# Performance work log

Hardware: AMD Instinct MI355X
Metric: run time of the kernel (lower is better)

The kernel has to match this reference:

```python
import jax, jax.numpy as jnp
import numpy as np

B, S, D = 46, 50, 768
GAMA = 1.0 - 2.0 ** -5  # 1 - np.power(2.0, -5 - arange(0,1)) -> scalar 0.96875


def make_pe(n, d):
    # PositionalEncoding buffer pe[:n]; note original adds pe[:emb.size(0)],
    # i.e. the encoding is indexed by BATCH position (faithful to source).
    position = jnp.arange(n, dtype=jnp.float32)[:, None]
    div_term = jnp.exp(jnp.arange(0, d, 2, dtype=jnp.float32) * (-np.log(10000.0) / d))
    pe = jnp.zeros((n, d), dtype=jnp.float32)
    pe = pe.at[:, 0::2].set(jnp.sin(position * div_term))
    pe = pe.at[:, 1::2].set(jnp.cos(position * div_term))
    return pe[:, None, :]  # [n, 1, d] broadcasts over the seq dim


def setup_inputs() -> dict:
    key = jax.random.key(0)
    ks = jax.random.split(key, 6)
    w = lambda k, shape: jax.random.normal(k, shape, dtype=jnp.float32) * 0.02
    return {
        "text_embedding": jax.random.normal(ks[0], (B, S, D), dtype=jnp.float32),
        "embedding": jax.random.normal(ks[1], (B, S, D), dtype=jnp.float32),
        "Wq_w": w(ks[2], (D, D)), "Wq_b": jnp.zeros((D,), jnp.float32),
        "Wk_w": w(ks[3], (D, D)), "Wk_b": jnp.zeros((D,), jnp.float32),
        "Wv_w": w(ks[4], (D, D)), "Wv_b": jnp.zeros((D,), jnp.float32),
        "lin_w": w(ks[5], (S, D)), "lin_b": jnp.zeros((S,), jnp.float32),
    }


def reference(text_embedding, embedding, Wq_w, Wq_b, Wk_w, Wk_b, Wv_w, Wv_b, lin_w, lin_b):
    b = text_embedding.shape[0]
    pe = make_pe(b, D)  # [B,1,D]
    # dropout p=0.1 is identity in eval mode
    Q = text_embedding @ Wq_w.T + Wq_b + pe          # [B,S,D]
    K = embedding @ Wk_w.T + Wk_b + pe               # [B,S,D]
    V = embedding @ Wv_w.T + Wv_b                    # [B,S,D]
    # head_num == 1, so transpose_for_scores is a no-op view
    Q_trans = Q @ lin_w.T + lin_b                    # [B,S,S] (S == 50)
    scores = jnp.einsum('bqd,bkd->bqk', Q, K) * 8.0  # scaling *8 as in source
    probs = jax.nn.softmax(scores, axis=-1)
    ctx = jnp.einsum('bqk,bkd->bqd', probs, V)       # [B,S,D] context_layer

    # RetNet-like gamma-decay recurrence over the batch dim (host-sync loop in
    # the original, expressed here as an on-device lax.scan):
    #   s_i = Q_trans @ (gama * s_{i-1}) + ctx[i],  s_{-1} = 0
    def step(s, c_i):  # s: [B,S,D], c_i: [S,D]
        s_new = jnp.einsum('bij,bjd->bid', Q_trans, GAMA * s) + c_i[None]
        return s_new, s_new
    _, rec = jax.lax.scan(step, jnp.zeros_like(ctx), ctx)  # [B,B,S,D]
    return ctx, rec
```

## Files before the change

### kernel.cpp

```cpp
#include <hip/hip_runtime.h>
#include <math.h>

#define NB 46
#define NS 50
#define ND 768
#define GAMA 0.96875f
#define NM 2300

using bfrag  = __attribute__((ext_vector_type(8))) short;
using f32x16 = __attribute__((ext_vector_type(16))) float;

union FragU { unsigned u[4]; bfrag f; };

__device__ __forceinline__ void cvt_hilo(const float f[8], bfrag& fh, bfrag& fl)
{
    FragU uh, ul;
    #pragma unroll
    for (int t = 0; t < 4; t++) {
        const unsigned b0 = __float_as_uint(f[2 * t]);
        const unsigned b1 = __float_as_uint(f[2 * t + 1]);
        uh.u[t] = (b0 >> 16) | (b1 & 0xFFFF0000u);
        const float r0 = f[2 * t]     - __uint_as_float(b0 & 0xFFFF0000u);
        const float r1 = f[2 * t + 1] - __uint_as_float(b1 & 0xFFFF0000u);
        ul.u[t] = (__float_as_uint(r0) >> 16) | (__float_as_uint(r1) & 0xFFFF0000u);
    }
    fh = uh.f; fl = ul.f;
}

__global__ __launch_bounds__(256) void qkv_gemm(
    const float* __restrict__ text_emb, const float* __restrict__ emb,
    const float* __restrict__ Wq, const float* __restrict__ bq,
    const float* __restrict__ Wk, const float* __restrict__ bk,
    const float* __restrict__ Wv, const float* __restrict__ bv,
    float* __restrict__ Q, float* __restrict__ K, float* __restrict__ V)
{
    const int z = blockIdx.z;
    const float* X    = (z == 0) ? text_emb : emb;
    const float* W    = (z == 0) ? Wq : (z == 1) ? Wk : Wv;
    const float* bias = (z == 0) ? bq : (z == 1) ? bk : bv;
    float* out        = (z == 0) ? Q  : (z == 1) ? K  : V;

    __shared__ float Xs[32][68];
    __shared__ float Ws[32][68];

    const int tid = threadIdx.x;
    const int w   = tid >> 6;
    const int l   = tid & 63;
    const int c   = l & 31;
    const int h   = l >> 5;
    const int wm  = w >> 1, wn = w & 1;
    const int m0  = blockIdx.x * 64, n0 = blockIdx.y * 64;

    const int lrow = tid >> 2;
    const int lk   = (tid & 3) * 4;
    const int xm   = m0 + lrow;
    const float* __restrict__ Xrow = X + (size_t)(xm < NM ? xm : 0) * ND;
    const float* __restrict__ Wrow = W + (size_t)(n0 + lrow) * ND;

    f32x16 acc;
    #pragma unroll
    for (int g = 0; g < 16; g++) acc[g] = 0.f;

    for (int k0 = 0; k0 < ND; k0 += 32) {
        const float4 xv0 = *reinterpret_cast<const float4*>(&Xrow[k0 + lk]);
        const float4 xv1 = *reinterpret_cast<const float4*>(&Xrow[k0 + 16 + lk]);
        const float4 wv0 = *reinterpret_cast<const float4*>(&Wrow[k0 + lk]);
        const float4 wv1 = *reinterpret_cast<const float4*>(&Wrow[k0 + 16 + lk]);
        __syncthreads();
        Xs[lk + 0][lrow] = xv0.x; Xs[lk + 1][lrow] = xv0.y;
        Xs[lk + 2][lrow] = xv0.z; Xs[lk + 3][lrow] = xv0.w;
        Xs[16 + lk + 0][lrow] = xv1.x; Xs[16 + lk + 1][lrow] = xv1.y;
        Xs[16 + lk + 2][lrow] = xv1.z; Xs[16 + lk + 3][lrow] = xv1.w;
        Ws[lk + 0][lrow] = wv0.x; Ws[lk + 1][lrow] = wv0.y;
        Ws[lk + 2][lrow] = wv0.z; Ws[lk + 3][lrow] = wv0.w;
        Ws[16 + lk + 0][lrow] = wv1.x; Ws[16 + lk + 1][lrow] = wv1.y;
        Ws[16 + lk + 2][lrow] = wv1.z; Ws[16 + lk + 3][lrow] = wv1.w;
        __syncthreads();

        #pragma unroll
        for (int kt = 0; kt < 2; kt++) {
            float fx[8], fw[8];
            #pragma unroll
            for (int j = 0; j < 8; j++) {
                fx[j] = Xs[16 * kt + 8 * h + j][32 * wm + c];
                fw[j] = Ws[16 * kt + 8 * h + j][32 * wn + c];
            }
            bfrag Ah, Al, Bh, Bl;
            cvt_hilo(fx, Ah, Al);
            cvt_hilo(fw, Bh, Bl);
            acc = __builtin_amdgcn_mfma_f32_32x32x16_bf16(Ah, Bh, acc, 0, 0, 0);
            acc = __builtin_amdgcn_mfma_f32_32x32x16_bf16(Ah, Bl, acc, 0, 0, 0);
            acc = __builtin_amdgcn_mfma_f32_32x32x16_bf16(Al, Bh, acc, 0, 0, 0);
        }
    }

    const float C2 = -0.0239861701969175f;
    const int n = n0 + 32 * wn + c;
    #pragma unroll
    for (int g = 0; g < 16; g++) {
        const int rr = (g & 3) + 8 * (g >> 2) + 4 * h;
        const int m  = m0 + 32 * wm + rr;
        if (m >= NM) continue;
        float v = acc[g] + bias[n];
        if (z < 2) {
            const int bpos = m / NS;
            const float ang = (float)bpos * expf((float)(n >> 1) * C2);
            v += (n & 1) ? cosf(ang) : sinf(ang);
        }
        out[(size_t)m * ND + n] = v;
    }
}

__global__ __launch_bounds__(256, 1) void attn(
    const float* __restrict__ Q, const float* __restrict__ K,
    const float* __restrict__ V,
    const float* __restrict__ lin_w, const float* __restrict__ lin_b,
    float* __restrict__ Ag, float* __restrict__ ctx_out)
{
    const int b   = blockIdx.x;
    const int tid = threadIdx.x;
    const int w   = tid >> 6;
    const int l   = tid & 63;
    const int c   = l & 31;
    const int h   = l >> 5;

    __shared__ float Lsh[9 * 64 * 68];
    float* SP = Lsh;
    float* QP = Lsh + 4 * 64 * 68;
    float* Pf = Lsh + 8 * 64 * 68;

    const float* __restrict__ Qb = Q + (size_t)b * NS * ND;
    const float* __restrict__ Kb = K + (size_t)b * NS * ND;
    const float* __restrict__ Vb = V + (size_t)b * NS * ND;

    f32x16 accS[2][2], accQ[2][2];
    #pragma unroll
    for (int mt = 0; mt < 2; mt++)
        #pragma unroll
        for (int nt = 0; nt < 2; nt++)
            #pragma unroll
            for (int g = 0; g < 16; g++) { accS[mt][nt][g] = 0.f; accQ[mt][nt][g] = 0.f; }

    const int ks = w * 192;
    for (int kt = 0; kt < 12; ++kt) {
        const int ko = ks + kt * 16 + 8 * h;
        bfrag Qh[2], Ql[2], Kh[2], Kl[2], Wh[2], Wl[2];
        #pragma unroll
        for (int mt = 0; mt < 2; mt++) {
            const int row = 32 * mt + c;
            const int r = (row < NS) ? row : 0;
            float f[8];
            {
                const float4 a0 = *reinterpret_cast<const float4*>(&Qb[(size_t)r * ND + ko]);
                const float4 a1 = *reinterpret_cast<const float4*>(&Qb[(size_t)r * ND + ko + 4]);
                f[0]=a0.x; f[1]=a0.y; f[2]=a0.z; f[3]=a0.w; f[4]=a1.x; f[5]=a1.y; f[6]=a1.z; f[7]=a1.w;
            }
            cvt_hilo(f, Qh[mt], Ql[mt]);
            {
                const float4 a0 = *reinterpret_cast<const float4*>(&Kb[(size_t)r * ND + ko]);
                const float4 a1 = *reinterpret_cast<const float4*>(&Kb[(size_t)r * ND + ko + 4]);
                f[0]=a0.x; f[1]=a0.y; f[2]=a0.z; f[3]=a0.w; f[4]=a1.x; f[5]=a1.y; f[6]=a1.z; f[7]=a1.w;
            }
            cvt_hilo(f, Kh[mt], Kl[mt]);
            {
                const float4 a0 = *reinterpret_cast<const float4*>(&lin_w[(size_t)r * ND + ko]);
                const float4 a1 = *reinterpret_cast<const float4*>(&lin_w[(size_t)r * ND + ko + 4]);
                f[0]=a0.x; f[1]=a0.y; f[2]=a0.z; f[3]=a0.w; f[4]=a1.x; f[5]=a1.y; f[6]=a1.z; f[7]=a1.w;
            }
            cvt_hilo(f, Wh[mt], Wl[mt]);
        }
        #pragma unroll
        for (int mt = 0; mt < 2; mt++)
            #pragma unroll
            for (int nt = 0; nt < 2; nt++) {
                f32x16 a = accS[mt][nt];
                a = __builtin_amdgcn_mfma_f32_32x32x16_bf16(Qh[mt], Kh[nt], a, 0, 0, 0);
                a = __builtin_amdgcn_mfma_f32_32x32x16_bf16(Qh[mt], Kl[nt], a, 0, 0, 0);
                a = __builtin_amdgcn_mfma_f32_32x32x16_bf16(Ql[mt], Kh[nt], a, 0, 0, 0);
                accS[mt][nt] = a;
                f32x16 q = accQ[mt][nt];
                q = __builtin_amdgcn_mfma_f32_32x32x16_bf16(Qh[mt], Wh[nt], q, 0, 0, 0);
                q = __builtin_amdgcn_mfma_f32_32x32x16_bf16(Qh[mt], Wl[nt], q, 0, 0, 0);
                q = __builtin_amdgcn_mfma_f32_32x32x16_bf16(Ql[mt], Wh[nt], q, 0, 0, 0);
                accQ[mt][nt] = q;
            }
    }

    {
        float* SPw = SP + w * (64 * 68);
        float* QPw = QP + w * (64 * 68);
        #pragma unroll
        for (int mt = 0; mt < 2; mt++)
            #pragma unroll
            for (int nt = 0; nt < 2; nt++)
                #pragma unroll
                for (int g = 0; g < 16; g++) {
                    const int rg  = 32 * mt + (g & 3) + 8 * (g >> 2) + 4 * h;
                    const int col = 32 * nt + c;
                    SPw[rg * 68 + col] = accS[mt][nt][g];
                    QPw[rg * 68 + col] = accQ[mt][nt][g];
                }
    }
    __syncthreads();

    {
        const int r  = tid >> 2;
        const int cg = (tid & 3) * 16;
        #pragma unroll
        for (int q4 = 0; q4 < 4; ++q4) {
            const int off = r * 68 + cg + q4 * 4;
            float4 s0 = *reinterpret_cast<const float4*>(&SP[off]);
            float4 s1 = *reinterpret_cast<const float4*>(&SP[64 * 68 + off]);
            float4 s2 = *reinterpret_cast<const float4*>(&SP[2 * 64 * 68 + off]);
            float4 s3 = *reinterpret_cast<const float4*>(&SP[3 * 64 * 68 + off]);
            float4 r4;
            r4.x = 8.f * ((s0.x + s1.x) + (s2.x + s3.x));
            r4.y = 8.f * ((s0.y + s1.y) + (s2.y + s3.y));
            r4.z = 8.f * ((s0.z + s1.z) + (s2.z + s3.z));
            r4.w = 8.f * ((s0.w + s1.w) + (s2.w + s3.w));
            *reinterpret_cast<float4*>(&SP[off]) = r4;
            float4 t0 = *reinterpret_cast<const float4*>(&QP[off]);
            float4 t1 = *reinterpret_cast<const float4*>(&QP[64 * 68 + off]);
            float4 t2 = *reinterpret_cast<const float4*>(&QP[2 * 64 * 68 + off]);
            float4 t3 = *reinterpret_cast<const float4*>(&QP[3 * 64 * 68 + off]);
            float4 u4;
            u4.x = (t0.x + t1.x) + (t2.x + t3.x);
            u4.y = (t0.y + t1.y) + (t2.y + t3.y);
            u4.z = (t0.z + t1.z) + (t2.z + t3.z);
            u4.w = (t0.w + t1.w) + (t2.w + t3.w);
            *reinterpret_cast<float4*>(&QP[off]) = u4;
        }
    }
    __syncthreads();

    if (tid < NS) {
        const float* Sr = SP + tid * 68;
        float mx = -INFINITY;
        for (int c2 = 0; c2 < NS; ++c2) mx = fmaxf(mx, Sr[c2]);
        float sum = 0.f;
        for (int c2 = 0; c2 < NS; ++c2) {
            const float e = expf(Sr[c2] - mx);
            Pf[tid * 68 + c2] = e;
            sum += e;
        }
        const float inv = 1.f / sum;
        for (int c2 = 0; c2 < NS; ++c2) Pf[tid * 68 + c2] *= inv;
        for (int c2 = NS; c2 < 64; ++c2) Pf[tid * 68 + c2] = 0.f;
    }
    for (int e = tid; e < NS * NS; e += 256) {
        const int r = e / NS, cc = e - r * NS;
        Ag[b * (NS * NS) + e] = GAMA * (QP[r * 68 + cc] + lin_b[cc]);
    }
    __syncthreads();

    bfrag Ph[2][4], Pl[2][4];
    #pragma unroll
    for (int mt = 0; mt < 2; mt++)
        #pragma unroll
        for (int kt = 0; kt < 4; kt++) {
            float f[8];
            #pragma unroll
            for (int j = 0; j < 8; j++)
                f[j] = Pf[(32 * mt + c) * 68 + kt * 16 + 8 * h + j];
            cvt_hilo(f, Ph[mt][kt], Pl[mt][kt]);
        }

    for (int j3 = 0; j3 < 3; ++j3) {
        const int dbase = (w * 3 + j3) * 64;
        f32x16 accC[2][2];
        #pragma unroll
        for (int mt = 0; mt < 2; mt++)
            #pragma unroll
            for (int nt = 0; nt < 2; nt++)
                #pragma unroll
                for (int g = 0; g < 16; g++) accC[mt][nt][g] = 0.f;

        #pragma unroll
        for (int nt = 0; nt < 2; nt++) {
            const int d = dbase + 32 * nt + c;
            #pragma unroll
            for (int kt = 0; kt < 4; kt++) {
                float f[8];
                #pragma unroll
                for (int j = 0; j < 8; j++) {
                    const int k2 = kt * 16 + 8 * h + j;
                    f[j] = (k2 < NS) ? Vb[(size_t)k2 * ND + d] : 0.f;
                }
                bfrag Bh, Bl;
                cvt_hilo(f, Bh, Bl);
                #pragma unroll
                for (int mt = 0; mt < 2; mt++) {
                    f32x16 a = accC[mt][nt];
                    a = __builtin_amdgcn_mfma_f32_32x32x16_bf16(Ph[mt][kt], Bh, a, 0, 0, 0);
                    a = __builtin_amdgcn_mfma_f32_32x32x16_bf16(Ph[mt][kt], Bl, a, 0, 0, 0);
                    a = __builtin_amdgcn_mfma_f32_32x32x16_bf16(Pl[mt][kt], Bh, a, 0, 0, 0);
                    accC[mt][nt] = a;
                }
            }
        }
        #pragma unroll
        for (int mt = 0; mt < 2; mt++)
            #pragma unroll
            for (int nt = 0; nt < 2; nt++)
                #pragma unroll
                for (int g = 0; g < 16; g++) {
                    const int rg = 32 * mt + (g & 3) + 8 * (g >> 2) + 4 * h;
                    if (rg < NS)
                        ctx_out[((size_t)b * NS + rg) * ND + dbase + 32 * nt + c] = accC[mt][nt][g];
                }
    }
}

__global__ __launch_bounds__(64, 1) void recur(
    const float* __restrict__ Ag, const float* __restrict__ ctx,
    float* __restrict__ rec)
{
    const int blk   = blockIdx.x;
    const int b     = blk / 24;
    const int chunk = blk - b * 24;
    const int l     = threadIdx.x;
    const int c     = l & 31;
    const int h     = l >> 5;
    const int d0    = chunk * 32;
    const int srow  = l >> 3;
    const int scol  = (l & 7) * 4;

    __shared__ float Sf[64 * 32];
    __shared__ float Cx[64 * 32];

    const float* __restrict__ Ab = Ag + b * (NS * NS);
    bfrag Ah[2][4], Al[2][4];
    #pragma unroll
    for (int mt = 0; mt < 2; mt++) {
        const int row = 32 * mt + c;
        const bool rok = row < NS;
        const float* __restrict__ Arow = Ab + row * NS;
        #pragma unroll
        for (int kt = 0; kt < 4; kt++) {
            FragU uh, ul;
            #pragma unroll
            for (int t = 0; t < 4; t++) {
                const int k0 = 16 * kt + 8 * h + 2 * t;
                const float e = (rok && k0     < NS) ? Arow[k0]     : 0.f;
                const float o = (rok && k0 + 1 < NS) ? Arow[k0 + 1] : 0.f;
                const unsigned ue = __float_as_uint(e), uo = __float_as_uint(o);
                uh.u[t] = (ue >> 16) | (uo & 0xFFFF0000u);
                const float re = e - __uint_as_float(ue & 0xFFFF0000u);
                const float ro = o - __uint_as_float(uo & 0xFFFF0000u);
                ul.u[t] = (__float_as_uint(re) >> 16) | (__float_as_uint(ro) & 0xFFFF0000u);
            }
            Ah[mt][kt] = uh.f; Al[mt][kt] = ul.f;
        }
    }

    {
        const float4 z = make_float4(0.f, 0.f, 0.f, 0.f);
        *reinterpret_cast<float4*>(&Cx[(48 + srow) * 32 + scol]) = z;
        *reinterpret_cast<float4*>(&Cx[(56 + srow) * 32 + scol]) = z;
        *reinterpret_cast<float4*>(&Sf[(48 + srow) * 32 + scol]) = z;
        *reinterpret_cast<float4*>(&Sf[(56 + srow) * 32 + scol]) = z;
    }

    float4 creg[7];
    #pragma unroll
    for (int it = 0; it < 7; ++it) creg[it] = make_float4(0.f, 0.f, 0.f, 0.f);
    {
        const float* __restrict__ src = ctx + d0;
        #pragma unroll
        for (int it = 0; it < 7; ++it) {
            const int r = it * 8 + srow;
            if (r < NS)
                creg[it] = *reinterpret_cast<const float4*>(&src[(size_t)r * ND + scol]);
        }
        float* __restrict__ r0 = rec + (size_t)b * NS * ND + d0;
        #pragma unroll
        for (int it = 0; it < 7; ++it) {
            const int r = it * 8 + srow;
            if (r < NS) {
                *reinterpret_cast<float4*>(&Sf[r * 32 + scol]) = creg[it];
                *reinterpret_cast<float4*>(&r0[(size_t)r * ND + scol]) = creg[it];
            }
        }
    }
    {
        const float* __restrict__ src = ctx + (size_t)NS * ND + d0;
        #pragma unroll
        for (int it = 0; it < 7; ++it) {
            const int r = it * 8 + srow;
            if (r < NS)
                creg[it] = *reinterpret_cast<const float4*>(&src[(size_t)r * ND + scol]);
        }
    }

    for (int i = 1; i < NB; ++i) {
        #pragma unroll
        for (int it = 0; it < 7; ++it) {
            const int r = it * 8 + srow;
            if (r < NS)
                *reinterpret_cast<float4*>(&Cx[r * 32 + scol]) = creg[it];
        }
        if (i + 1 < NB) {
            const float* __restrict__ src = ctx + (size_t)(i + 1) * NS * ND + d0;
            #pragma unroll
            for (int it = 0; it < 7; ++it) {
                const int r = it * 8 + srow;
                if (r < NS)
                    creg[it] = *reinterpret_cast<const float4*>(&src[(size_t)r * ND + scol]);
            }
        }
        f32x16 acc[2];
        #pragma unroll
        for (int mt = 0; mt < 2; mt++)
            #pragma unroll
            for (int g = 0; g < 16; g++) {
                const int rg = 32 * mt + (g & 3) + 8 * (g >> 2) + 4 * h;
                acc[mt][g] = Cx[rg * 32 + c];
            }
        bfrag Bh[4], Bl[4];
        #pragma unroll
        for (int kt = 0; kt < 4; kt++) {
            float f[8];
            #pragma unroll
            for (int j = 0; j < 8; j++)
                f[j] = Sf[(16 * kt + 8 * h + j) * 32 + c];
            FragU uh, ul;
            #pragma unroll
            for (int t = 0; t < 4; t++) {
                const unsigned b0 = __float_as_uint(f[2 * t]);
                const unsigned b1 = __float_as_uint(f[2 * t + 1]);
                uh.u[t] = (b0 >> 16) | (b1 & 0xFFFF0000u);
                const float r0f = f[2 * t]     - __uint_as_float(b0 & 0xFFFF0000u);
                const float r1f = f[2 * t + 1] - __uint_as_float(b1 & 0xFFFF0000u);
                ul.u[t] = (__float_as_uint(r0f) >> 16) | (__float_as_uint(r1f) & 0xFFFF0000u);
            }
            Bh[kt] = uh.f; Bl[kt] = ul.f;
        }
        #pragma unroll
        for (int mt = 0; mt < 2; mt++) {
            f32x16 a = acc[mt];
            #pragma unroll
            for (int kt = 0; kt < 4; kt++)
                a = __builtin_amdgcn_mfma_f32_32x32x16_bf16(Ah[mt][kt], Bh[kt], a, 0, 0, 0);
            #pragma unroll
            for (int kt = 0; kt < 4; kt++)
                a = __builtin_amdgcn_mfma_f32_32x32x16_bf16(Ah[mt][kt], Bl[kt], a, 0, 0, 0);
            #pragma unroll
            for (int kt = 0; kt < 4; kt++)
                a = __builtin_amdgcn_mfma_f32_32x32x16_bf16(Al[mt][kt], Bh[kt], a, 0, 0, 0);
            acc[mt] = a;
        }
        #pragma unroll
        for (int mt = 0; mt < 2; mt++)
            #pragma unroll
            for (int g = 0; g < 16; g++) {
                const int rg = 32 * mt + (g & 3) + 8 * (g >> 2) + 4 * h;
                Sf[rg * 32 + c] = acc[mt][g];
            }
        float* __restrict__ reci = rec + (size_t)(i * NB + b) * NS * ND + d0;
        #pragma unroll
        for (int it = 0; it < 7; ++it) {
            const int r = it * 8 + srow;
            if (r < NS) {
                const float4 v = *reinterpret_cast<const float4*>(&Sf[r * 32 + scol]);
                *reinterpret_cast<float4*>(&reci[(size_t)r * ND + scol]) = v;
            }
        }
    }
}

extern "C" void kernel_launch(void* const* d_in, const int* in_sizes, int n_in,
                              void* d_out, int out_size, void* d_ws, size_t ws_size,
                              hipStream_t stream) {
    const float* text_emb = (const float*)d_in[0];
    const float* emb      = (const float*)d_in[1];
    const float* Wq = (const float*)d_in[2]; const float* bq = (const float*)d_in[3];
    const float* Wk = (const float*)d_in[4]; const float* bk = (const float*)d_in[5];
    const float* Wv = (const float*)d_in[6]; const float* bv = (const float*)d_in[7];
    const float* lw = (const float*)d_in[8]; const float* lb = (const float*)d_in[9];

    float* out = (float*)d_out;
    float* ctx = out;
    float* rec = out + NB * NS * ND;

    float* ws = (float*)d_ws;
    float* Q  = ws;
    float* K  = Q + NB * NS * ND;
    float* V  = K + NB * NS * ND;
    float* Ag = V + NB * NS * ND;

    qkv_gemm<<<dim3(36, 12, 3), 256, 0, stream>>>(text_emb, emb, Wq, bq, Wk, bk, Wv, bv, Q, K, V);
    attn<<<dim3(NB), 256, 0, stream>>>(Q, K, V, lw, lb, Ag, ctx);
    recur<<<dim3(1104), 64, 0, stream>>>(Ag, ctx, rec);
}
```

Baseline: 189.4 us.

## Split recurrence blocks across two waves with double-buffered state

Each recurrence block now runs two wavefronts instead of one, each owning one 32-row M tile of the per-batch 50x50 matrix. That halves the serial chain of MFMAs and the LDS traffic per wave at every time step. The state buffer is ping-ponged between two LDS arrays so each step needs only one workgroup barrier. The cost is a barrier per step and more LDS per block, while occupancy rises through launch bounds of (128, 2).

```diff
diff --git a/kernel.cpp b/kernel.cpp
--- a/kernel.cpp
+++ b/kernel.cpp
@@ -311,28 +311,89 @@
     }
 }
 
-__global__ __launch_bounds__(64, 1) void recur(
+__device__ __forceinline__ void rec2_step(
+    int i, int b, int d0, int c, int h, int wid, int srow, int scol,
+    const bfrag (&Ah)[4], const bfrag (&Al)[4],
+    float4 (&creg)[4],
+    const float* SfR, float* SfW, float* Cx,
+    const float* __restrict__ ctx, float* __restrict__ rec)
+{
+    #pragma unroll
+    for (int it = 0; it < 4; ++it) {
+        const int r = (4 * wid + it) * 8 + srow;
+        if (r < NS)
+            *reinterpret_cast<float4*>(&Cx[r * 32 + scol]) = creg[it];
+    }
+    if (i + 1 < NB) {
+        const float* __restrict__ src = ctx + (size_t)(i + 1) * NS * ND + d0;
+        #pragma unroll
+        for (int it = 0; it < 4; ++it) {
+            const int r = (4 * wid + it) * 8 + srow;
+            if (r < NS)
+                creg[it] = *reinterpret_cast<const float4*>(&src[(size_t)r * ND + scol]);
+        }
+    }
+    f32x16 acc;
+    #pragma unroll
+    for (int g = 0; g < 16; g++) {
+        const int rg = 32 * wid + (g & 3) + 8 * (g >> 2) + 4 * h;
+        acc[g] = Cx[rg * 32 + c];
+    }
+    #pragma unroll
+    for (int kt = 0; kt < 4; kt++) {
+        float f[8];
+        #pragma unroll
+        for (int j = 0; j < 8; j++)
+            f[j] = SfR[(16 * kt + 8 * h + j) * 32 + c];
+        bfrag Bh, Bl;
+        cvt_hilo(f, Bh, Bl);
+        acc = __builtin_amdgcn_mfma_f32_32x32x16_bf16(Ah[kt], Bh, acc, 0, 0, 0);
+        acc = __builtin_amdgcn_mfma_f32_32x32x16_bf16(Ah[kt], Bl, acc, 0, 0, 0);
+        acc = __builtin_amdgcn_mfma_f32_32x32x16_bf16(Al[kt], Bh, acc, 0, 0, 0);
+    }
+    #pragma unroll
+    for (int g = 0; g < 16; g++) {
+        const int rg = 32 * wid + (g & 3) + 8 * (g >> 2) + 4 * h;
+        SfW[rg * 32 + c] = acc[g];
+    }
+    float* __restrict__ reci = rec + (size_t)(i * NB + b) * NS * ND + d0;
+    #pragma unroll
+    for (int it = 0; it < 4; ++it) {
+        const int r = (4 * wid + it) * 8 + srow;
+        if (r < NS) {
+            const float4 v = *reinterpret_cast<const float4*>(&SfW[r * 32 + scol]);
+            *reinterpret_cast<float4*>(&reci[(size_t)r * ND + scol]) = v;
+        }
+    }
+    asm volatile("s_waitcnt lgkmcnt(0)" ::: "memory");
+    __builtin_amdgcn_s_barrier();
+    asm volatile("" ::: "memory");
+}
+
+__global__ __launch_bounds__(128, 2) void recur(
     const float* __restrict__ Ag, const float* __restrict__ ctx,
     float* __restrict__ rec)
 {
     const int blk   = blockIdx.x;
     const int b     = blk / 24;
     const int chunk = blk - b * 24;
-    const int l     = threadIdx.x;
+    const int tid   = threadIdx.x;
+    const int wid   = tid >> 6;
+    const int l     = tid & 63;
     const int c     = l & 31;
     const int h     = l >> 5;
     const int d0    = chunk * 32;
     const int srow  = l >> 3;
     const int scol  = (l & 7) * 4;
 
-    __shared__ float Sf[64 * 32];
-    __shared__ float Cx[64 * 32];
+    __shared__ float Sfa[64 * 32];
+    __shared__ float Sfb[64 * 32];
+    __shared__ float Cx [64 * 32];
 
     const float* __restrict__ Ab = Ag + b * (NS * NS);
-    bfrag Ah[2][4], Al[2][4];
-    #pragma unroll
-    for (int mt = 0; mt < 2; mt++) {
-        const int row = 32 * mt + c;
+    bfrag Ah[4], Al[4];
+    {
+        const int row = 32 * wid + c;
         const bool rok = row < NS;
         const float* __restrict__ Arow = Ab + row * NS;
         #pragma unroll
@@ -349,123 +410,57 @@
                 const float ro = o - __uint_as_float(uo & 0xFFFF0000u);
                 ul.u[t] = (__float_as_uint(re) >> 16) | (__float_as_uint(ro) & 0xFFFF0000u);
             }
-            Ah[mt][kt] = uh.f; Al[mt][kt] = ul.f;
-        }
-    }
-
-    {
-        const float4 z = make_float4(0.f, 0.f, 0.f, 0.f);
-        *reinterpret_cast<float4*>(&Cx[(48 + srow) * 32 + scol]) = z;
-        *reinterpret_cast<float4*>(&Cx[(56 + srow) * 32 + scol]) = z;
-        *reinterpret_cast<float4*>(&Sf[(48 + srow) * 32 + scol]) = z;
-        *reinterpret_cast<float4*>(&Sf[(56 + srow) * 32 + scol]) = z;
-    }
-
-    float4 creg[7];
-    #pragma unroll
-    for (int it = 0; it < 7; ++it) creg[it] = make_float4(0.f, 0.f, 0.f, 0.f);
+            Ah[kt] = uh.f; Al[kt] = ul.f;
+        }
+    }
+
+    for (int idx = tid; idx < 14 * 32; idx += 128) {
+        const int rr = 50 + (idx >> 5), cc = idx & 31;
+        Cx [rr * 32 + cc] = 0.f;
+        Sfa[rr * 32 + cc] = 0.f;
+    }
+
+    float4 creg[4];
+    #pragma unroll
+    for (int it = 0; it < 4; ++it) creg[it] = make_float4(0.f, 0.f, 0.f, 0.f);
     {
         const float* __restrict__ src = ctx + d0;
-        #pragma unroll
-        for (int it = 0; it < 7; ++it) {
-            const int r = it * 8 + srow;
+        float4 c0[4];
+        #pragma unroll
+        for (int it = 0; it < 4; ++it) {
+            c0[it] = make_float4(0.f, 0.f, 0.f, 0.f);
+            const int r = (4 * wid + it) * 8 + srow;
             if (r < NS)
-                creg[it] = *reinterpret_cast<const float4*>(&src[(size_t)r * ND + scol]);
+                c0[it] = *reinterpret_cast<const float4*>(&src[(size_t)r * ND + scol]);
+        }
+        const float* __restrict__ s1 = ctx + (size_t)NS * ND + d0;
+        #pragma unroll
+        for (int it = 0; it < 4; ++it) {
+            const int r = (4 * wid + it) * 8 + srow;
+            if (r < NS)
+                creg[it] = *reinterpret_cast<const float4*>(&s1[(size_t)r * ND + scol]);
         }
         float* __restrict__ r0 = rec + (size_t)b * NS * ND + d0;
         #pragma unroll
-        for (int it = 0; it < 7; ++it) {
-            const int r = it * 8 + srow;
+        for (int it = 0; it < 4; ++it) {
+            const int r = (4 * wid + it) * 8 + srow;
             if (r < NS) {
-                *reinterpret_cast<float4*>(&Sf[r * 32 + scol]) = creg[it];
-                *reinterpret_cast<float4*>(&r0[(size_t)r * ND + scol]) = creg[it];
-            }
-        }
-    }
-    {
-        const float* __restrict__ src = ctx + (size_t)NS * ND + d0;
-        #pragma unroll
-        for (int it = 0; it < 7; ++it) {
-            const int r = it * 8 + srow;
-            if (r < NS)
-                creg[it] = *reinterpret_cast<const float4*>(&src[(size_t)r * ND + scol]);
-        }
-    }
-
-    for (int i = 1; i < NB; ++i) {
-        #pragma unroll
-        for (int it = 0; it < 7; ++it) {
-            const int r = it * 8 + srow;
-            if (r < NS)
-                *reinterpret_cast<float4*>(&Cx[r * 32 + scol]) = creg[it];
-        }
-        if (i + 1 < NB) {
-            const float* __restrict__ src = ctx + (size_t)(i + 1) * NS * ND + d0;
-            #pragma unroll
-            for (int it = 0; it < 7; ++it) {
-                const int r = it * 8 + srow;
-                if (r < NS)
-                    creg[it] = *reinterpret_cast<const float4*>(&src[(size_t)r * ND + scol]);
-            }
-        }
-        f32x16 acc[2];
-        #pragma unroll
-        for (int mt = 0; mt < 2; mt++)
-            #pragma unroll
-            for (int g = 0; g < 16; g++) {
-                const int rg = 32 * mt + (g & 3) + 8 * (g >> 2) + 4 * h;
-                acc[mt][g] = Cx[rg * 32 + c];
-            }
-        bfrag Bh[4], Bl[4];
-        #pragma unroll
-        for (int kt = 0; kt < 4; kt++) {
-            float f[8];
-            #pragma unroll
-            for (int j = 0; j < 8; j++)
-                f[j] = Sf[(16 * kt + 8 * h + j) * 32 + c];
-            FragU uh, ul;
-            #pragma unroll
-            for (int t = 0; t < 4; t++) {
-                const unsigned b0 = __float_as_uint(f[2 * t]);
-                const unsigned b1 = __float_as_uint(f[2 * t + 1]);
-                uh.u[t] = (b0 >> 16) | (b1 & 0xFFFF0000u);
-                const float r0f = f[2 * t]     - __uint_as_float(b0 & 0xFFFF0000u);
-                const float r1f = f[2 * t + 1] - __uint_as_float(b1 & 0xFFFF0000u);
-                ul.u[t] = (__float_as_uint(r0f) >> 16) | (__float_as_uint(r1f) & 0xFFFF0000u);
-            }
-            Bh[kt] = uh.f; Bl[kt] = ul.f;
-        }
-        #pragma unroll
-        for (int mt = 0; mt < 2; mt++) {
-            f32x16 a = acc[mt];
-            #pragma unroll
-            for (int kt = 0; kt < 4; kt++)
-                a = __builtin_amdgcn_mfma_f32_32x32x16_bf16(Ah[mt][kt], Bh[kt], a, 0, 0, 0);
-            #pragma unroll
-            for (int kt = 0; kt < 4; kt++)
-                a = __builtin_amdgcn_mfma_f32_32x32x16_bf16(Ah[mt][kt], Bl[kt], a, 0, 0, 0);
-            #pragma unroll
-            for (int kt = 0; kt < 4; kt++)
-                a = __builtin_amdgcn_mfma_f32_32x32x16_bf16(Al[mt][kt], Bh[kt], a, 0, 0, 0);
-            acc[mt] = a;
-        }
-        #pragma unroll
-        for (int mt = 0; mt < 2; mt++)
-            #pragma unroll
-            for (int g = 0; g < 16; g++) {
-                const int rg = 32 * mt + (g & 3) + 8 * (g >> 2) + 4 * h;
-                Sf[rg * 32 + c] = acc[mt][g];
-            }
-        float* __restrict__ reci = rec + (size_t)(i * NB + b) * NS * ND + d0;
-        #pragma unroll
-        for (int it = 0; it < 7; ++it) {
-            const int r = it * 8 + srow;
-            if (r < NS) {
-                const float4 v = *reinterpret_cast<const float4*>(&Sf[r * 32 + scol]);
-                *reinterpret_cast<float4*>(&reci[(size_t)r * ND + scol]) = v;
-            }
-        }
-    }
+                *reinterpret_cast<float4*>(&Sfa[r * 32 + scol]) = c0[it];
+                *reinterpret_cast<float4*>(&r0[(size_t)r * ND + scol]) = c0[it];
+            }
+        }
+    }
+    asm volatile("s_waitcnt lgkmcnt(0)" ::: "memory");
+    __builtin_amdgcn_s_barrier();
+    asm volatile("" ::: "memory");
+
+    int i = 1;
+    for (; i + 1 < NB; i += 2) {
+        rec2_step(i,     b, d0, c, h, wid, srow, scol, Ah, Al, creg, Sfa, Sfb, Cx, ctx, rec);
+        rec2_step(i + 1, b, d0, c, h, wid, srow, scol, Ah, Al, creg, Sfb, Sfa, Cx, ctx, rec);
+    }
+    if (i < NB)
+        rec2_step(i, b, d0, c, h, wid, srow, scol, Ah, Al, creg, Sfa, Sfb, Cx, ctx, rec);
 }
 
 extern "C" void kernel_launch(void* const* d_in, const int* in_sizes, int n_in,
@@ -490,5 +485,5 @@
 
     qkv_gemm<<<dim3(36, 12, 3), 256, 0, stream>>>(text_emb, emb, Wq, bq, Wk, bk, Wv, bv, Q, K, V);
     attn<<<dim3(NB), 256, 0, stream>>>(Q, K, V, lw, lb, Ag, ctx);
-    recur<<<dim3(1104), 64, 0, stream>>>(Ag, ctx, rec);
-}
+    recur<<<dim3(1104), 128, 0, stream>>>(Ag, ctx, rec);
+}
```

Measured after the change: 206.0 us. +8.7%, slower.
